# Performance work log

Measured on AMD Instinct MI355X. Metric: run time of the kernel, lower is better.

## Reference

```python
import jax, jax.numpy as jnp
import numpy as np

DE_NEIGHBORS = 8

def _cdist(a, b):
    # a: [B,N,C], b: [B,S,C] -> [B,N,S] euclidean distance
    d2 = (jnp.sum(a * a, -1)[:, :, None] + jnp.sum(b * b, -1)[:, None, :]
          - 2.0 * jnp.einsum('bnc,bsc->bns', a, b))
    return jnp.sqrt(jnp.maximum(d2, 0.0))

def _propagate(xyz1, xyz2, n1, n2, p1, p2, k):
    # xyz1/n1: [B,N,3] fine; xyz2/n2: [B,S,3] coarse; p1: [B,N,C]; p2: [B,S,C]
    dists = _cdist(xyz1, xyz2) + jax.nn.sigmoid(_cdist(n1, n2))  # [B,N,S]
    negd, idx = jax.lax.top_k(-dists, k)                         # k smallest
    d = -negd
    recip = 1.0 / (d + 1e-8)
    w = recip / jnp.sum(recip, axis=-1, keepdims=True)           # [B,N,k]
    gathered = jax.vmap(lambda p, i: p[i])(p2, idx)              # [B,N,k,C]
    interp = jnp.einsum('bnkc,bnk->bnc', gathered, w)
    # cat=False merge: elementwise (max + mean)/2 of (p1, interp)
    return (jnp.maximum(p1, interp) + (p1 + interp) * 0.5) * 0.5

def setup_inputs() -> dict:
    key = jax.random.key(0)
    ks = jax.random.split(key, 12)
    Ns = [16384, 4096, 1024, 256]
    B, C = 2, 256
    out = {}
    for i, N in enumerate(Ns):
        out[f'xyz{i}'] = jax.random.normal(ks[i], (B, N, 3), jnp.float32)
        out[f'nrm{i}'] = jax.random.normal(ks[4 + i], (B, N, 3), jnp.float32)
        out[f'feat{i}'] = jax.random.normal(ks[8 + i], (B, N, C), jnp.float32)
    return out

def reference(xyz0, xyz1, xyz2, xyz3, nrm0, nrm1, nrm2, nrm3,
              feat0, feat1, feat2, feat3):
    # forward reverses the lists: index 0 = coarsest
    xyzs = [xyz3, xyz2, xyz1, xyz0]
    nrms = [nrm3, nrm2, nrm1, nrm0]
    pts = [feat3, feat2, feat1, feat0]
    x = pts[0]
    for i in range(3):  # num_stages
        x = _propagate(xyzs[i + 1], xyzs[i], nrms[i + 1], nrms[i],
                       pts[i + 1], x, DE_NEIGHBORS)
    return x
```

## Files before the change

kernel.cpp:

```cpp
#include <hip/hip_runtime.h>

#define KNBR 8

__global__ __launch_bounds__(256) void pack_kernel(
    const float* __restrict__ xa, const float* __restrict__ na, int ca,
    const float* __restrict__ xb, const float* __restrict__ nb, int cb,
    const float* __restrict__ xc, const float* __restrict__ nc_, int cc,
    float* __restrict__ pa, float* __restrict__ pb, float* __restrict__ pc)
{
#pragma clang fp contract(off)
    int t = blockIdx.x * blockDim.x + threadIdx.x;
    const float* xs; const float* ns; float* dst; int i;
    if (t < ca)            { xs = xa; ns = na;  dst = pa; i = t; }
    else if (t < ca + cb)  { xs = xb; ns = nb;  dst = pb; i = t - ca; }
    else if (t < ca+cb+cc) { xs = xc; ns = nc_; dst = pc; i = t - ca - cb; }
    else return;
    float x = xs[3*i], y = xs[3*i+1], z = xs[3*i+2];
    float u = ns[3*i], v = ns[3*i+1], w = ns[3*i+2];
    float4 r0 = make_float4(-2.f*x, -2.f*y, -2.f*z, (x*x + y*y) + z*z);
    float4 r1 = make_float4(-2.f*u, -2.f*v, -2.f*w, (u*u + v*v) + w*w);
    reinterpret_cast<float4*>(dst)[2*i]     = r0;
    reinterpret_cast<float4*>(dst)[2*i + 1] = r1;
}

#define CEX(V, I, A, B) { bool sw_ = V[B] < V[A];                       \
    float lo_ = sw_ ? V[B] : V[A]; float hi_ = sw_ ? V[A] : V[B];       \
    int   li_ = sw_ ? I[B] : I[A]; int   hj_ = sw_ ? I[A] : I[B];       \
    V[A] = lo_; V[B] = hi_; I[A] = li_; I[B] = hj_; }

template<int L>
__device__ __forceinline__ void topk_body(
    int vblk, const float* __restrict__ xyzF, const float* __restrict__ nrmF,
    const float* __restrict__ packC, int NF, int NC,
    int* __restrict__ outIdx, float* __restrict__ outW)
{
    const int lane = threadIdx.x & (L - 1);
    const int grp  = (vblk * 256 + (int)threadIdx.x) / L;
    const int b    = grp >= NF ? 1 : 0;

    const float* fp = xyzF + (size_t)grp * 3;
    float fx = fp[0], fy = fp[1], fz = fp[2];
    const float* gp = nrmF + (size_t)grp * 3;
    float gx = gp[0], gy = gp[1], gz = gp[2];
    float sax = fmaf(fx, fx, fmaf(fy, fy, fz * fz));
    float san = fmaf(gx, gx, fmaf(gy, gy, gz * gz));

    float d[KNBR]; int id[KNBR];
#pragma unroll
    for (int j = 0; j < KNBR; ++j) { d[j] = 3.402823466e38f; id[j] = 0; }

    const float4* base = reinterpret_cast<const float4*>(packC) + (size_t)b * NC * 2;
    const int nch = NC / (8 * L);
    for (int cc = 0; cc < nch; ++cc) {
        const int s0 = cc * (8 * L) + lane;
        const float4* p = base + (size_t)s0 * 2;
        float4 q0[8], q1[8];
#pragma unroll
        for (int k = 0; k < 8; ++k) { q0[k] = p[2*L*k]; q1[k] = p[2*L*k + 1]; }

        float cv[8]; int ci[8];
#pragma unroll
        for (int k = 0; k < 8; ++k) {
            float d2  = fmaf(fx, q0[k].x, fmaf(fy, q0[k].y,
                        fmaf(fz, q0[k].z, sax + q0[k].w)));
            float dxx = __builtin_amdgcn_sqrtf(fmaxf(d2, 0.0f));
            float d2n = fmaf(gx, q1[k].x, fmaf(gy, q1[k].y,
                        fmaf(gz, q1[k].z, san + q1[k].w)));
            float dnn = __builtin_amdgcn_sqrtf(fmaxf(d2n, 0.0f));
            float sg  = __builtin_amdgcn_rcpf(1.0f + __expf(-dnn));
            cv[k] = dxx + sg;
            ci[k] = s0 + k * L;
        }

        CEX(cv,ci,0,1) CEX(cv,ci,2,3) CEX(cv,ci,4,5) CEX(cv,ci,6,7)
        CEX(cv,ci,0,2) CEX(cv,ci,1,3) CEX(cv,ci,4,6) CEX(cv,ci,5,7)
        CEX(cv,ci,1,2) CEX(cv,ci,5,6)
        CEX(cv,ci,0,4) CEX(cv,ci,1,5) CEX(cv,ci,2,6) CEX(cv,ci,3,7)
        CEX(cv,ci,2,4) CEX(cv,ci,3,5)
        CEX(cv,ci,1,2) CEX(cv,ci,3,4) CEX(cv,ci,5,6)

        float nd[KNBR]; int ni[KNBR];
#pragma unroll
        for (int i = 0; i < KNBR; ++i) {
            bool t = cv[KNBR-1-i] < d[i];
            nd[i] = t ? cv[KNBR-1-i] : d[i];
            ni[i] = t ? ci[KNBR-1-i] : id[i];
        }
        CEX(nd,ni,0,4) CEX(nd,ni,1,5) CEX(nd,ni,2,6) CEX(nd,ni,3,7)
        CEX(nd,ni,0,2) CEX(nd,ni,1,3) CEX(nd,ni,4,6) CEX(nd,ni,5,7)
        CEX(nd,ni,0,1) CEX(nd,ni,2,3) CEX(nd,ni,4,5) CEX(nd,ni,6,7)
#pragma unroll
        for (int j = 0; j < KNBR; ++j) { d[j] = nd[j]; id[j] = ni[j]; }
    }

#pragma unroll
    for (int m = 1; m < L; m <<= 1) {
        float pd[KNBR]; int pi[KNBR];
#pragma unroll
        for (int j = 0; j < KNBR; ++j) {
            pd[j] = __shfl_xor(d[j], m);
            pi[j] = __shfl_xor(id[j], m);
        }
        float nd[KNBR]; int ni[KNBR];
#pragma unroll
        for (int j = 0; j < KNBR; ++j) {
            bool t = pd[KNBR-1-j] < d[j];
            nd[j] = t ? pd[KNBR-1-j] : d[j];
            ni[j] = t ? pi[KNBR-1-j] : id[j];
        }
        CEX(nd,ni,0,4) CEX(nd,ni,1,5) CEX(nd,ni,2,6) CEX(nd,ni,3,7)
        CEX(nd,ni,0,2) CEX(nd,ni,1,3) CEX(nd,ni,4,6) CEX(nd,ni,5,7)
        CEX(nd,ni,0,1) CEX(nd,ni,2,3) CEX(nd,ni,4,5) CEX(nd,ni,6,7)
#pragma unroll
        for (int j = 0; j < KNBR; ++j) { d[j] = nd[j]; id[j] = ni[j]; }
    }

    if (lane == 0) {
        float r[KNBR]; float sum = 0.f;
#pragma unroll
        for (int j = 0; j < KNBR; ++j) { r[j] = 1.0f / (d[j] + 1e-8f); sum += r[j]; }
        int*   oi = outIdx + (size_t)grp * KNBR;
        float* ow = outW   + (size_t)grp * KNBR;
#pragma unroll
        for (int j = 0; j < KNBR; ++j) { oi[j] = id[j]; ow[j] = r[j] / sum; }
    }
}

#define G2 2048
#define G1 512
#define G0 128
__global__ __launch_bounds__(256) void topk_fused(
    const float* __restrict__ xyz0, const float* __restrict__ nrm0,
    const float* __restrict__ xyz1, const float* __restrict__ nrm1,
    const float* __restrict__ xyz2, const float* __restrict__ nrm2,
    const float* __restrict__ pack1, const float* __restrict__ pack2,
    const float* __restrict__ pack3,
    int* __restrict__ idx2, float* __restrict__ w2,
    int* __restrict__ idx1, float* __restrict__ w1,
    int* __restrict__ idx0, float* __restrict__ w0)
{
    const int blk = blockIdx.x;
    if (blk < G2)
        topk_body<16>(blk, xyz0, nrm0, pack1, 16384, 4096, idx2, w2);
    else if (blk < G2 + G1)
        topk_body<16>(blk - G2, xyz1, nrm1, pack2, 4096, 1024, idx1, w1);
    else
        topk_body<16>(blk - G2 - G1, xyz2, nrm2, pack3, 1024, 256, idx0, w0);
}

__global__ __launch_bounds__(256) void interp_kernel(
    const float* __restrict__ p1, const float* __restrict__ p2,
    const int* __restrict__ idx, const float* __restrict__ w,
    int NF, int NC, float* __restrict__ out)
{
    const int pt = blockIdx.x * 4 + (threadIdx.x >> 6);
    const int c4 = threadIdx.x & 63;
    const int b  = pt >= NF ? 1 : 0;
    const int*   ip = idx + (size_t)pt * KNBR;
    const float* wp = w   + (size_t)pt * KNBR;
    const float4* p2b = reinterpret_cast<const float4*>(p2) + (size_t)b * NC * 64;
    float4 acc = make_float4(0.f, 0.f, 0.f, 0.f);
#pragma unroll
    for (int j = 0; j < KNBR; ++j) {
        int   ii = ip[j];
        float ww = wp[j];
        float4 r = p2b[(size_t)ii * 64 + c4];
        acc.x += ww * r.x; acc.y += ww * r.y;
        acc.z += ww * r.z; acc.w += ww * r.w;
    }
    float4 a = reinterpret_cast<const float4*>(p1)[(size_t)pt * 64 + c4];
    float4 o;
    o.x = (fmaxf(a.x, acc.x) + (a.x + acc.x) * 0.5f) * 0.5f;
    o.y = (fmaxf(a.y, acc.y) + (a.y + acc.y) * 0.5f) * 0.5f;
    o.z = (fmaxf(a.z, acc.z) + (a.z + acc.z) * 0.5f) * 0.5f;
    o.w = (fmaxf(a.w, acc.w) + (a.w + acc.w) * 0.5f) * 0.5f;
    reinterpret_cast<float4*>(out)[(size_t)pt * 64 + c4] = o;
}

extern "C" void kernel_launch(void* const* d_in, const int* in_sizes, int n_in,
                              void* d_out, int out_size, void* d_ws, size_t ws_size,
                              hipStream_t stream)
{
    const float* xyz0  = (const float*)d_in[0];
    const float* nrm0  = (const float*)d_in[1];
    const float* feat0 = (const float*)d_in[2];
    const float* xyz1  = (const float*)d_in[3];
    const float* nrm1  = (const float*)d_in[4];
    const float* feat1 = (const float*)d_in[5];
    const float* xyz2  = (const float*)d_in[6];
    const float* nrm2  = (const float*)d_in[7];
    const float* feat2 = (const float*)d_in[8];
    const float* xyz3  = (const float*)d_in[9];
    const float* nrm3  = (const float*)d_in[10];
    const float* feat3 = (const float*)d_in[11];

    const int B = 2, C = 256;
    const int N0 = 16384, N1 = 4096, N2 = 1024, N3 = 256;

    float* ws = (float*)d_ws;
    size_t off = 0;
    float* pack1 = ws + off; off += (size_t)B*N1*8;
    float* pack2 = ws + off; off += (size_t)B*N2*8;
    float* pack3 = ws + off; off += (size_t)B*N3*8;
    int*   idx0  = (int*)(ws + off); off += (size_t)B*N2*KNBR;
    float* w0    = ws + off;         off += (size_t)B*N2*KNBR;
    int*   idx1  = (int*)(ws + off); off += (size_t)B*N1*KNBR;
    float* w1    = ws + off;         off += (size_t)B*N1*KNBR;
    int*   idx2  = (int*)(ws + off); off += (size_t)B*N0*KNBR;
    float* w2    = ws + off;         off += (size_t)B*N0*KNBR;
    float* x0    = ws + off;         off += (size_t)B*N2*C;
    float* x1    = ws + off;         off += (size_t)B*N1*C;

    int packTot = B * (N1 + N2 + N3);
    pack_kernel<<<(packTot + 255)/256, 256, 0, stream>>>(
        xyz1, nrm1, B*N1, xyz2, nrm2, B*N2, xyz3, nrm3, B*N3,
        pack1, pack2, pack3);

    topk_fused<<<G2 + G1 + G0, 256, 0, stream>>>(
        xyz0, nrm0, xyz1, nrm1, xyz2, nrm2,
        pack1, pack2, pack3, idx2, w2, idx1, w1, idx0, w0);

    interp_kernel<<<(B*N2)/4, 256, 0, stream>>>(feat2, feat3, idx0, w0, N2, N3, x0);
    interp_kernel<<<(B*N1)/4, 256, 0, stream>>>(feat1, x0,    idx1, w1, N1, N2, x1);
    interp_kernel<<<(B*N0)/4, 256, 0, stream>>>(feat0, x1,    idx2, w2, N0, N1, (float*)d_out);
}
```

Measured before the change: 291.0 us.

## Stage coarse points in LDS and pack candidate slot into quantized distance keys

```diff
diff --git a/kernel.cpp b/kernel.cpp
--- a/kernel.cpp
+++ b/kernel.cpp
@@ -23,20 +23,25 @@
     reinterpret_cast<float4*>(dst)[2*i + 1] = r1;
 }
 
-#define CEX(V, I, A, B) { bool sw_ = V[B] < V[A];                       \
-    float lo_ = sw_ ? V[B] : V[A]; float hi_ = sw_ ? V[A] : V[B];       \
-    int   li_ = sw_ ? I[B] : I[A]; int   hj_ = sw_ ? I[A] : I[B];       \
+#define CEXU(V, I, A, B) { bool sw_ = V[B] < V[A];                        \
+    unsigned lo_ = sw_ ? V[B] : V[A]; unsigned hi_ = sw_ ? V[A] : V[B];   \
+    int li_ = sw_ ? I[B] : I[A]; int hj_ = sw_ ? I[A] : I[B];             \
     V[A] = lo_; V[B] = hi_; I[A] = li_; I[B] = hj_; }
 
-template<int L>
-__device__ __forceinline__ void topk_body(
+#define CEXVU(V, A, B) { unsigned lo_ = min(V[A], V[B]);                  \
+    unsigned hi_ = max(V[A], V[B]); V[A] = lo_; V[B] = hi_; }
+
+__device__ __forceinline__ void topk_body16(
     int vblk, const float* __restrict__ xyzF, const float* __restrict__ nrmF,
     const float* __restrict__ packC, int NF, int NC,
-    int* __restrict__ outIdx, float* __restrict__ outW)
-{
-    const int lane = threadIdx.x & (L - 1);
-    const int grp  = (vblk * 256 + (int)threadIdx.x) / L;
+    int* __restrict__ outIdx, float* __restrict__ outW,
+    float4* sbuf )
+{
+    const int tid  = (int)threadIdx.x;
+    const int lane = tid & 15;
+    const int grp  = (vblk * 256 + tid) >> 4;
     const int b    = grp >= NF ? 1 : 0;
+    const int sl = tid & 63, w = tid >> 6, h = w & 1, g = w >> 1;
 
     const float* fp = xyzF + (size_t)grp * 3;
     float fx = fp[0], fy = fp[1], fz = fp[2];
@@ -45,84 +50,101 @@
     float sax = fmaf(fx, fx, fmaf(fy, fy, fz * fz));
     float san = fmaf(gx, gx, fmaf(gy, gy, gz * gz));
 
-    float d[KNBR]; int id[KNBR];
-#pragma unroll
-    for (int j = 0; j < KNBR; ++j) { d[j] = 3.402823466e38f; id[j] = 0; }
-
-    const float4* base = reinterpret_cast<const float4*>(packC) + (size_t)b * NC * 2;
-    const int nch = NC / (8 * L);
+    unsigned d[KNBR]; int ib[KNBR];
+#pragma unroll
+    for (int j = 0; j < KNBR; ++j) { d[j] = 0xFFFFFFFFu; ib[j] = 0; }
+
+    const float4* pc4 = reinterpret_cast<const float4*>(packC) + (size_t)b * NC * 2;
+    const int nch = NC >> 7;
+
+    sbuf[h * 128 + g * 64 + sl] = pc4[(size_t)(g * 64 + sl) * 2 + h];
+    __syncthreads();
+
+    int cur = 0;
     for (int cc = 0; cc < nch; ++cc) {
-        const int s0 = cc * (8 * L) + lane;
-        const float4* p = base + (size_t)s0 * 2;
-        float4 q0[8], q1[8];
-#pragma unroll
-        for (int k = 0; k < 8; ++k) { q0[k] = p[2*L*k]; q1[k] = p[2*L*k + 1]; }
-
-        float cv[8]; int ci[8];
+        float4 st;
+        const bool do_stage = (cc + 1 < nch);
+        if (do_stage)
+            st = pc4[(size_t)((cc + 1) * 128 + g * 64 + sl) * 2 + h];
+
+        const float4* bq = sbuf + cur * 256;
+        const int s0 = cc * 128 + lane;
+        unsigned cv[8];
 #pragma unroll
         for (int k = 0; k < 8; ++k) {
-            float d2  = fmaf(fx, q0[k].x, fmaf(fy, q0[k].y,
-                        fmaf(fz, q0[k].z, sax + q0[k].w)));
+            float4 c0 = bq[lane + k * 16];
+            float4 c1 = bq[128 + lane + k * 16];
+            float d2  = fmaf(fx, c0.x, fmaf(fy, c0.y, fmaf(fz, c0.z, sax + c0.w)));
             float dxx = __builtin_amdgcn_sqrtf(fmaxf(d2, 0.0f));
-            float d2n = fmaf(gx, q1[k].x, fmaf(gy, q1[k].y,
-                        fmaf(gz, q1[k].z, san + q1[k].w)));
+            float d2n = fmaf(gx, c1.x, fmaf(gy, c1.y, fmaf(gz, c1.z, san + c1.w)));
             float dnn = __builtin_amdgcn_sqrtf(fmaxf(d2n, 0.0f));
             float sg  = __builtin_amdgcn_rcpf(1.0f + __expf(-dnn));
-            cv[k] = dxx + sg;
-            ci[k] = s0 + k * L;
-        }
-
-        CEX(cv,ci,0,1) CEX(cv,ci,2,3) CEX(cv,ci,4,5) CEX(cv,ci,6,7)
-        CEX(cv,ci,0,2) CEX(cv,ci,1,3) CEX(cv,ci,4,6) CEX(cv,ci,5,7)
-        CEX(cv,ci,1,2) CEX(cv,ci,5,6)
-        CEX(cv,ci,0,4) CEX(cv,ci,1,5) CEX(cv,ci,2,6) CEX(cv,ci,3,7)
-        CEX(cv,ci,2,4) CEX(cv,ci,3,5)
-        CEX(cv,ci,1,2) CEX(cv,ci,3,4) CEX(cv,ci,5,6)
-
-        float nd[KNBR]; int ni[KNBR];
+            float v   = dxx + sg;
+            unsigned u = (unsigned)(v * 134217728.0f);
+            cv[k] = u | (unsigned)k;
+        }
+
+        CEXVU(cv,0,1) CEXVU(cv,2,3) CEXVU(cv,4,5) CEXVU(cv,6,7)
+        CEXVU(cv,0,2) CEXVU(cv,1,3) CEXVU(cv,4,6) CEXVU(cv,5,7)
+        CEXVU(cv,1,2) CEXVU(cv,5,6)
+        CEXVU(cv,0,4) CEXVU(cv,1,5) CEXVU(cv,2,6) CEXVU(cv,3,7)
+        CEXVU(cv,2,4) CEXVU(cv,3,5)
+        CEXVU(cv,1,2) CEXVU(cv,3,4) CEXVU(cv,5,6)
+
+        unsigned nd[KNBR]; int ni[KNBR];
 #pragma unroll
         for (int i = 0; i < KNBR; ++i) {
             bool t = cv[KNBR-1-i] < d[i];
             nd[i] = t ? cv[KNBR-1-i] : d[i];
-            ni[i] = t ? ci[KNBR-1-i] : id[i];
-        }
-        CEX(nd,ni,0,4) CEX(nd,ni,1,5) CEX(nd,ni,2,6) CEX(nd,ni,3,7)
-        CEX(nd,ni,0,2) CEX(nd,ni,1,3) CEX(nd,ni,4,6) CEX(nd,ni,5,7)
-        CEX(nd,ni,0,1) CEX(nd,ni,2,3) CEX(nd,ni,4,5) CEX(nd,ni,6,7)
-#pragma unroll
-        for (int j = 0; j < KNBR; ++j) { d[j] = nd[j]; id[j] = ni[j]; }
-    }
-
-#pragma unroll
-    for (int m = 1; m < L; m <<= 1) {
-        float pd[KNBR]; int pi[KNBR];
+            ni[i] = t ? s0 : ib[i];
+        }
+        CEXU(nd,ni,0,4) CEXU(nd,ni,1,5) CEXU(nd,ni,2,6) CEXU(nd,ni,3,7)
+        CEXU(nd,ni,0,2) CEXU(nd,ni,1,3) CEXU(nd,ni,4,6) CEXU(nd,ni,5,7)
+        CEXU(nd,ni,0,1) CEXU(nd,ni,2,3) CEXU(nd,ni,4,5) CEXU(nd,ni,6,7)
+#pragma unroll
+        for (int j = 0; j < KNBR; ++j) { d[j] = nd[j]; ib[j] = ni[j]; }
+
+        if (do_stage)
+            sbuf[(cur ^ 1) * 256 + h * 128 + g * 64 + sl] = st;
+        __syncthreads();
+        cur ^= 1;
+    }
+
+#pragma unroll
+    for (int m = 1; m < 16; m <<= 1) {
+        unsigned pd[KNBR]; int pi[KNBR];
 #pragma unroll
         for (int j = 0; j < KNBR; ++j) {
-            pd[j] = __shfl_xor(d[j], m);
-            pi[j] = __shfl_xor(id[j], m);
-        }
-        float nd[KNBR]; int ni[KNBR];
+            pd[j] = (unsigned)__shfl_xor((int)d[j], m);
+            pi[j] = __shfl_xor(ib[j], m);
+        }
+        unsigned nd[KNBR]; int ni[KNBR];
 #pragma unroll
         for (int j = 0; j < KNBR; ++j) {
             bool t = pd[KNBR-1-j] < d[j];
             nd[j] = t ? pd[KNBR-1-j] : d[j];
-            ni[j] = t ? pi[KNBR-1-j] : id[j];
-        }
-        CEX(nd,ni,0,4) CEX(nd,ni,1,5) CEX(nd,ni,2,6) CEX(nd,ni,3,7)
-        CEX(nd,ni,0,2) CEX(nd,ni,1,3) CEX(nd,ni,4,6) CEX(nd,ni,5,7)
-        CEX(nd,ni,0,1) CEX(nd,ni,2,3) CEX(nd,ni,4,5) CEX(nd,ni,6,7)
-#pragma unroll
-        for (int j = 0; j < KNBR; ++j) { d[j] = nd[j]; id[j] = ni[j]; }
+            ni[j] = t ? pi[KNBR-1-j] : ib[j];
+        }
+        CEXU(nd,ni,0,4) CEXU(nd,ni,1,5) CEXU(nd,ni,2,6) CEXU(nd,ni,3,7)
+        CEXU(nd,ni,0,2) CEXU(nd,ni,1,3) CEXU(nd,ni,4,6) CEXU(nd,ni,5,7)
+        CEXU(nd,ni,0,1) CEXU(nd,ni,2,3) CEXU(nd,ni,4,5) CEXU(nd,ni,6,7)
+#pragma unroll
+        for (int j = 0; j < KNBR; ++j) { d[j] = nd[j]; ib[j] = ni[j]; }
     }
 
     if (lane == 0) {
         float r[KNBR]; float sum = 0.f;
-#pragma unroll
-        for (int j = 0; j < KNBR; ++j) { r[j] = 1.0f / (d[j] + 1e-8f); sum += r[j]; }
+        int   ix[KNBR];
+#pragma unroll
+        for (int j = 0; j < KNBR; ++j) {
+            float v = (float)(d[j] & ~7u) * 7.450580596923828e-9f;
+            ix[j] = ib[j] + (int)(d[j] & 7u) * 16;
+            r[j] = 1.0f / (v + 1e-8f); sum += r[j];
+        }
         int*   oi = outIdx + (size_t)grp * KNBR;
         float* ow = outW   + (size_t)grp * KNBR;
 #pragma unroll
-        for (int j = 0; j < KNBR; ++j) { oi[j] = id[j]; ow[j] = r[j] / sum; }
+        for (int j = 0; j < KNBR; ++j) { oi[j] = ix[j]; ow[j] = r[j] / sum; }
     }
 }
 
@@ -139,13 +161,14 @@
     int* __restrict__ idx1, float* __restrict__ w1,
     int* __restrict__ idx0, float* __restrict__ w0)
 {
+    __shared__ float4 sbuf[2 * 256];
     const int blk = blockIdx.x;
     if (blk < G2)
-        topk_body<16>(blk, xyz0, nrm0, pack1, 16384, 4096, idx2, w2);
+        topk_body16(blk, xyz0, nrm0, pack1, 16384, 4096, idx2, w2, sbuf);
     else if (blk < G2 + G1)
-        topk_body<16>(blk - G2, xyz1, nrm1, pack2, 4096, 1024, idx1, w1);
+        topk_body16(blk - G2, xyz1, nrm1, pack2, 4096, 1024, idx1, w1, sbuf);
     else
-        topk_body<16>(blk - G2 - G1, xyz2, nrm2, pack3, 1024, 256, idx0, w0);
+        topk_body16(blk - G2 - G1, xyz2, nrm2, pack3, 1024, 256, idx0, w0, sbuf);
 }
 
 __global__ __launch_bounds__(256) void interp_kernel(
```

Measured after the change: 276.6 us. 5.0% less time.
